# Kernel tuning notes

Measured on AMD Instinct MI355X. Metric: run time of the kernel, lower is better.

The kernel has to match this reference:

```python
import jax, jax.numpy as jnp
import numpy as np

U, V, A = 100000, 50000, 5000   # n_users, n_videos, n_vloggers
D = 64                           # latent_dim_rec
N_LAYERS = 3                     # VAGNN_n_layers
NNZ_UI, NNZ_UA, NNZ_G2, NNZ_G4 = 4_000_000, 2_000_000, 200_000, 2_000_000
BATCH = 1024

def spmm(rows, cols, vals, x, n_rows):
    # sparse.mm(COO(rows, cols, vals), x) -> [n_rows, d]
    return jax.ops.segment_sum(vals[:, None] * x[cols], rows, num_segments=n_rows)

def one_propagate(rows, cols, vals, a_feat, b_feat):
    # LightGCN propagation: mean over layer-0..n embeddings (running sum, no stack)
    n = a_feat.shape[0] + b_feat.shape[0]
    feats = jnp.concatenate([a_feat, b_feat], axis=0)
    acc, cur = feats, feats
    for _ in range(N_LAYERS):
        cur = spmm(rows, cols, vals, cur, n)
        acc = acc + cur
    light = acc / (N_LAYERS + 1)
    return light[:a_feat.shape[0]], light[a_feat.shape[0]:]

def l2norm(x):
    # F.normalize(x, dim=1), eps=1e-12
    return x / jnp.maximum(jnp.linalg.norm(x, axis=1, keepdims=True), 1e-12)

def setup_inputs() -> dict:
    key = jax.random.key(0)
    ks = jax.random.split(key, 16)
    return {
        'emb_user':    jax.random.normal(ks[0], (U, D), jnp.float32) * 0.1,
        'emb_video':   jax.random.normal(ks[1], (V, D), jnp.float32) * 0.1,
        'emb_vlogger': jax.random.normal(ks[2], (A, D), jnp.float32) * 0.1,
        'q':           jax.random.normal(ks[3], (D, D), jnp.float32) * 0.1,
        'ui_rows': jax.random.randint(ks[4], (NNZ_UI,), 0, U + V, jnp.int32),
        'ui_cols': jax.random.randint(ks[5], (NNZ_UI,), 0, U + V, jnp.int32),
        'ui_vals': jax.random.uniform(ks[6], (NNZ_UI,), jnp.float32) * 0.01,
        'ua_rows': jax.random.randint(ks[7], (NNZ_UA,), 0, U + A, jnp.int32),
        'ua_cols': jax.random.randint(ks[8], (NNZ_UA,), 0, U + A, jnp.int32),
        'ua_vals': jax.random.uniform(ks[9], (NNZ_UA,), jnp.float32) * 0.01,
        'g2_rows': jax.random.randint(ks[10], (NNZ_G2,), 0, A, jnp.int32),
        'g2_cols': jax.random.randint(ks[11], (NNZ_G2,), 0, V, jnp.int32),
        'g2_vals': jax.random.uniform(ks[12], (NNZ_G2,), jnp.float32) * 0.01,
        'g4_rows': jax.random.randint(ks[13], (NNZ_G4,), 0, V, jnp.int32),
        'g4_cols': jax.random.randint(ks[14], (NNZ_G4,), 0, U, jnp.int32),
        'g4_vals': jax.random.uniform(ks[15], (NNZ_G4,), jnp.float32) * 0.01,
        'vlogger_list': jax.random.randint(jax.random.fold_in(key, 100), (V,), 0, A, jnp.int32),
        'users': jax.random.randint(jax.random.fold_in(key, 101), (BATCH,), 0, U, jnp.int32),
    }

def reference(emb_user, emb_video, emb_vlogger, q,
              ui_rows, ui_cols, ui_vals,
              ua_rows, ua_cols, ua_vals,
              g2_rows, g2_cols, g2_vals,
              g4_rows, g4_cols, g4_vals,
              vlogger_list, users):
    # computer()
    atom_u, atom_v = one_propagate(ui_rows, ui_cols, ui_vals, emb_user, emb_video)
    atom_a = l2norm(spmm(g2_rows, g2_cols, g2_vals, atom_v, A))
    non_u, non_a = one_propagate(ua_rows, ua_cols, ua_vals, emb_user, emb_vlogger)
    non_v = l2norm(spmm(g4_rows, g4_cols, g4_vals, non_u, V))
    # getUsersRating()
    u_a, u_n = atom_u[users], non_u[users]                 # [B, D]
    vl_a, vl_n = atom_a[vlogger_list], non_a[vlogger_list]  # [V, D]
    ui = jax.nn.sigmoid(u_a @ atom_v.T + u_n @ non_v.T)      # [B, V]
    ua = jax.nn.sigmoid(u_a @ vl_a.T + u_n @ vl_n.T)         # [B, V]
    vid = (atom_v + non_v) * 0.5
    vlog = (vl_a + vl_n) * 0.5
    w = jax.nn.sigmoid(jnp.sum((vid @ q) * vlog, axis=1))    # [V]
    return w * ui + (1.0 - w) * ua
```

## Files before the change

kernel.cpp:

```cpp
#include <hip/hip_runtime.h>
#include <hip/hip_bf16.h>

#define U_N 100000
#define V_N 50000
#define A_N 5000

typedef float4 f4;
typedef unsigned int u32;
typedef __attribute__((ext_vector_type(8))) short bf16x8;
typedef __attribute__((ext_vector_type(4))) float f32x4;

__device__ inline float bflo(u32 p) { return __uint_as_float(p << 16); }
__device__ inline float bfhi(u32 p) { return __uint_as_float(p & 0xffff0000u); }
__device__ inline u32 f2bf(float f) {
  u32 u = __float_as_uint(f);
  return (u + 0x7fffu + ((u >> 16) & 1u)) >> 16;
}
__device__ inline u32 pack2(float lo, float hi) {
  return f2bf(lo) | (f2bf(hi) << 16);
}
__device__ inline bf16x8 ld8(const u32* p) {
  uint4 u = *(const uint4*)p;
  return __builtin_bit_cast(bf16x8, u);
}

__global__ void k_concat2b(const float* __restrict__ a, int na,
                           const float* __restrict__ b, int nb,
                           u32* __restrict__ curH, float* __restrict__ acc) {
  int total4 = (na + nb) * 16;
  for (int i = blockIdx.x * blockDim.x + threadIdx.x; i < total4;
       i += gridDim.x * blockDim.x) {
    int fi = i * 4;
    f4 v = (fi < na * 64) ? *(const f4*)(a + fi)
                          : *(const f4*)(b + (fi - na * 64));
    *(f4*)(acc + fi) = v;
    uint2 h; h.x = pack2(v.x, v.y); h.y = pack2(v.z, v.w);
    *(uint2*)(curH + (fi >> 1)) = h;
  }
}

__global__ void k_count(const int* __restrict__ rows, int nnz, int* __restrict__ cnt) {
  for (int i = blockIdx.x * blockDim.x + threadIdx.x; i < nnz;
       i += gridDim.x * blockDim.x)
    atomicAdd(&cnt[rows[i]], 1);
}

__global__ void k_bsum(const int* __restrict__ cnt, int n, int* __restrict__ bsum) {
  __shared__ int red[1024];
  int t = threadIdx.x;
  int i = blockIdx.x * 1024 + t;
  red[t] = (i < n) ? cnt[i] : 0;
  __syncthreads();
  for (int off = 512; off; off >>= 1) {
    if (t < off) red[t] += red[t + off];
    __syncthreads();
  }
  if (t == 0) bsum[blockIdx.x] = red[0];
}

__global__ void k_bscan(int* __restrict__ bsum, int nb) {
  if (threadIdx.x == 0) {
    int run = 0;
    for (int i = 0; i < nb; ++i) {
      int c = bsum[i];
      bsum[i] = run;
      run += c;
    }
  }
}

__global__ void k_bapply(const int* __restrict__ cnt, int n,
                         const int* __restrict__ bsum,
                         int* __restrict__ rp, int* __restrict__ pos) {
  __shared__ int sc[1024];
  int t = threadIdx.x;
  int i = blockIdx.x * 1024 + t;
  int c = (i < n) ? cnt[i] : 0;
  sc[t] = c;
  __syncthreads();
  #pragma unroll
  for (int off = 1; off < 1024; off <<= 1) {
    int v = (t >= off) ? sc[t - off] : 0;
    __syncthreads();
    sc[t] += v;
    __syncthreads();
  }
  int val = bsum[blockIdx.x] + sc[t] - c;
  if (i < n) {
    rp[i] = val;
    pos[i] = val;
    if (i == n - 1) rp[n] = val + c;
  }
}

__global__ void k_fill(const int* __restrict__ rows, const int* __restrict__ cols,
                       const float* __restrict__ vals, int nnz,
                       int* __restrict__ pos, int* __restrict__ ci,
                       float* __restrict__ cv) {
  for (int i = blockIdx.x * blockDim.x + threadIdx.x; i < nnz;
       i += gridDim.x * blockDim.x) {
    int slot = atomicAdd(&pos[rows[i]], 1);
    ci[slot] = cols[i];
    cv[slot] = vals[i];
  }
}

__global__ void k_spmm_b(const int* __restrict__ rp, const int* __restrict__ ci,
                         const float* __restrict__ cv, int nrows,
                         const u32* __restrict__ inH, int instrU,
                         u32* __restrict__ outH, int ostrU, int ocolU,
                         float* __restrict__ acc, int l2n) {
  int lane = threadIdx.x & 63;
  int w = (blockIdx.x * blockDim.x + threadIdx.x) >> 6;
  int nw = (gridDim.x * blockDim.x) >> 6;
  int eg = lane >> 3;
  int du = (lane & 7) * 4;
  for (int r = w; r < nrows; r += nw) {
    int e0 = rp[r], e1 = rp[r + 1];
    float s[8] = {0.f, 0.f, 0.f, 0.f, 0.f, 0.f, 0.f, 0.f};
    int e = e0 + eg;
    for (; e + 8 < e1; e += 16) {
      int c0 = ci[e];     float v0 = cv[e];
      int c1 = ci[e + 8]; float v1 = cv[e + 8];
      uint4 x0 = *(const uint4*)(inH + (size_t)c0 * instrU + du);
      uint4 x1 = *(const uint4*)(inH + (size_t)c1 * instrU + du);
      s[0] = fmaf(v0, bflo(x0.x), s[0]); s[1] = fmaf(v0, bfhi(x0.x), s[1]);
      s[2] = fmaf(v0, bflo(x0.y), s[2]); s[3] = fmaf(v0, bfhi(x0.y), s[3]);
      s[4] = fmaf(v0, bflo(x0.z), s[4]); s[5] = fmaf(v0, bfhi(x0.z), s[5]);
      s[6] = fmaf(v0, bflo(x0.w), s[6]); s[7] = fmaf(v0, bfhi(x0.w), s[7]);
      s[0] = fmaf(v1, bflo(x1.x), s[0]); s[1] = fmaf(v1, bfhi(x1.x), s[1]);
      s[2] = fmaf(v1, bflo(x1.y), s[2]); s[3] = fmaf(v1, bfhi(x1.y), s[3]);
      s[4] = fmaf(v1, bflo(x1.z), s[4]); s[5] = fmaf(v1, bfhi(x1.z), s[5]);
      s[6] = fmaf(v1, bflo(x1.w), s[6]); s[7] = fmaf(v1, bfhi(x1.w), s[7]);
    }
    if (e < e1) {
      int c0 = ci[e]; float v0 = cv[e];
      uint4 x0 = *(const uint4*)(inH + (size_t)c0 * instrU + du);
      s[0] = fmaf(v0, bflo(x0.x), s[0]); s[1] = fmaf(v0, bfhi(x0.x), s[1]);
      s[2] = fmaf(v0, bflo(x0.y), s[2]); s[3] = fmaf(v0, bfhi(x0.y), s[3]);
      s[4] = fmaf(v0, bflo(x0.z), s[4]); s[5] = fmaf(v0, bfhi(x0.z), s[5]);
      s[6] = fmaf(v0, bflo(x0.w), s[6]); s[7] = fmaf(v0, bfhi(x0.w), s[7]);
    }
    #pragma unroll
    for (int j = 0; j < 8; ++j) {
      s[j] += __shfl_xor(s[j], 8);
      s[j] += __shfl_xor(s[j], 16);
      s[j] += __shfl_xor(s[j], 32);
    }
    if (l2n) {
      float ss = 0.f;
      #pragma unroll
      for (int j = 0; j < 8; ++j) ss = fmaf(s[j], s[j], ss);
      ss += __shfl_xor(ss, 1);
      ss += __shfl_xor(ss, 2);
      ss += __shfl_xor(ss, 4);
      float inv = 1.0f / fmaxf(sqrtf(ss), 1e-12f);
      #pragma unroll
      for (int j = 0; j < 8; ++j) s[j] *= inv;
    }
    if (eg == 0) {
      uint4 o;
      o.x = pack2(s[0], s[1]); o.y = pack2(s[2], s[3]);
      o.z = pack2(s[4], s[5]); o.w = pack2(s[6], s[7]);
      *(uint4*)(outH + (size_t)r * ostrU + ocolU + du) = o;
      if (acc) {
        float* ap = acc + (size_t)r * 64 + (lane & 7) * 8;
        f4 a0 = *(f4*)ap, a1 = *(f4*)(ap + 4);
        a0.x += s[0]; a0.y += s[1]; a0.z += s[2]; a0.w += s[3];
        a1.x += s[4]; a1.y += s[5]; a1.z += s[6]; a1.w += s[7];
        *(f4*)ap = a0; *(f4*)(ap + 4) = a1;
      }
    }
  }
}

__global__ void k_scale_ua(float* __restrict__ acc, u32* __restrict__ UAuH) {
  int total4 = (U_N + A_N) * 16;
  for (int i = blockIdx.x * blockDim.x + threadIdx.x; i < total4;
       i += gridDim.x * blockDim.x) {
    int fi = i * 4;
    f4 v = *(f4*)(acc + fi);
    v.x *= 0.25f; v.y *= 0.25f; v.z *= 0.25f; v.w *= 0.25f;
    *(f4*)(acc + fi) = v;
    if (fi < U_N * 64) {
      uint2 h; h.x = pack2(v.x, v.y); h.y = pack2(v.z, v.w);
      *(uint2*)(UAuH + (fi >> 1)) = h;
    }
  }
}

__global__ void k_scale_ui(float* __restrict__ acc, u32* __restrict__ VAH) {
  int total4 = (U_N + V_N) * 16;
  for (int i = blockIdx.x * blockDim.x + threadIdx.x; i < total4;
       i += gridDim.x * blockDim.x) {
    int fi = i * 4;
    f4 v = *(f4*)(acc + fi);
    v.x *= 0.25f; v.y *= 0.25f; v.z *= 0.25f; v.w *= 0.25f;
    *(f4*)(acc + fi) = v;
    if (fi >= U_N * 64) {
      int rem = fi - U_N * 64;
      int row = rem >> 6, col = rem & 63;
      uint2 h; h.x = pack2(v.x, v.y); h.y = pack2(v.z, v.w);
      *(uint2*)(VAH + (size_t)row * 64 + (col >> 1)) = h;
    }
  }
}

__global__ void k_gather_u(const int* __restrict__ users,
                           const float* __restrict__ accUI,
                           const float* __restrict__ accUA,
                           u32* __restrict__ UcatH) {
  int b = blockIdx.x;
  int t = threadIdx.x;
  int u = users[b];
  UcatH[b * 64 + t] = pack2(accUI[(size_t)u * 64 + 2 * t], accUI[(size_t)u * 64 + 2 * t + 1]);
  UcatH[b * 64 + 32 + t] = pack2(accUA[(size_t)u * 64 + 2 * t], accUA[(size_t)u * 64 + 2 * t + 1]);
}

__global__ void k_gather_vb(const int* __restrict__ vlist,
                            const u32* __restrict__ atomAH,
                            const float* __restrict__ accUA,
                            u32* __restrict__ VBH) {
  int v = blockIdx.x * 4 + (threadIdx.x >> 5);
  int t = threadIdx.x & 31;
  int a = vlist[v];
  VBH[(size_t)v * 64 + t] = atomAH[(size_t)a * 32 + t];
  VBH[(size_t)v * 64 + 32 + t] =
      pack2(accUA[(size_t)(U_N + a) * 64 + 2 * t], accUA[(size_t)(U_N + a) * 64 + 2 * t + 1]);
}

__global__ void k_w(const u32* __restrict__ VAH, const u32* __restrict__ VBH,
                    const float* __restrict__ q, float* __restrict__ wv) {
  __shared__ float qs[64 * 64];
  for (int i = threadIdx.x; i < 4096; i += blockDim.x) qs[i] = q[i];
  __syncthreads();
  int lane = threadIdx.x & 63;
  int v = blockIdx.x * 4 + (threadIdx.x >> 6);
  if (v >= V_N) return;
  int half = lane & 1;
  u32 pa0 = VAH[(size_t)v * 64 + (lane >> 1)];
  u32 pa1 = VAH[(size_t)v * 64 + 32 + (lane >> 1)];
  u32 pb0 = VBH[(size_t)v * 64 + (lane >> 1)];
  u32 pb1 = VBH[(size_t)v * 64 + 32 + (lane >> 1)];
  float vid = 0.5f * ((half ? bfhi(pa0) : bflo(pa0)) + (half ? bfhi(pa1) : bflo(pa1)));
  float vlog = 0.5f * ((half ? bfhi(pb0) : bflo(pb0)) + (half ? bfhi(pb1) : bflo(pb1)));
  float s = 0.0f;
  for (int d = 0; d < 64; ++d)
    s = fmaf(__shfl(vid, d, 64), qs[d * 64 + lane], s);
  float t = s * vlog;
  #pragma unroll
  for (int off = 32; off; off >>= 1) t += __shfl_xor(t, off, 64);
  if (lane == 0) wv[v] = 1.0f / (1.0f + __expf(-t));
}

__global__ __launch_bounds__(256) void k_rating_mfma(
    const u32* __restrict__ UcatH, const u32* __restrict__ VAH,
    const u32* __restrict__ VBH, const float* __restrict__ wv,
    float* __restrict__ out) {
  int lane = threadIdx.x & 63;
  int wave = threadIdx.x >> 6;
  int n0 = blockIdx.x * 64;
  int m0 = blockIdx.y * 256 + wave * 64;
  int rr = lane & 15, g = lane >> 4;
  f32x4 accA[4][4], accB[4][4];
  #pragma unroll
  for (int i = 0; i < 4; ++i)
    #pragma unroll
    for (int j = 0; j < 4; ++j) {
      accA[i][j] = (f32x4){0.f, 0.f, 0.f, 0.f};
      accB[i][j] = (f32x4){0.f, 0.f, 0.f, 0.f};
    }
  #pragma unroll
  for (int ks = 0; ks < 4; ++ks) {
    int ko = ks * 16 + g * 4;
    bf16x8 a[4], bA[4], bB[4];
    #pragma unroll
    for (int i = 0; i < 4; ++i)
      a[i] = ld8(UcatH + (size_t)(m0 + i * 16 + rr) * 64 + ko);
    #pragma unroll
    for (int j = 0; j < 4; ++j) {
      int nr = n0 + j * 16 + rr;
      if (nr >= V_N) nr = V_N - 1;
      bA[j] = ld8(VAH + (size_t)nr * 64 + ko);
      bB[j] = ld8(VBH + (size_t)nr * 64 + ko);
    }
    #pragma unroll
    for (int i = 0; i < 4; ++i)
      #pragma unroll
      for (int j = 0; j < 4; ++j) {
        accA[i][j] = __builtin_amdgcn_mfma_f32_16x16x32_bf16(a[i], bA[j], accA[i][j], 0, 0, 0);
        accB[i][j] = __builtin_amdgcn_mfma_f32_16x16x32_bf16(a[i], bB[j], accB[i][j], 0, 0, 0);
      }
  }
  #pragma unroll
  for (int j = 0; j < 4; ++j) {
    int v = n0 + j * 16 + rr;
    if (v >= V_N) continue;
    float wvv = wv[v];
    #pragma unroll
    for (int i = 0; i < 4; ++i) {
      #pragma unroll
      for (int reg = 0; reg < 4; ++reg) {
        int u = m0 + i * 16 + g * 4 + reg;
        float sa = 1.0f / (1.0f + __expf(-accA[i][j][reg]));
        float sb = 1.0f / (1.0f + __expf(-accB[i][j][reg]));
        out[(size_t)u * V_N + v] = wvv * sa + (1.0f - wvv) * sb;
      }
    }
  }
}

extern "C" void kernel_launch(void* const* d_in, const int* in_sizes, int n_in,
                              void* d_out, int out_size, void* d_ws, size_t ws_size,
                              hipStream_t stream) {
  const float* emb_user    = (const float*)d_in[0];
  const float* emb_video   = (const float*)d_in[1];
  const float* emb_vlogger = (const float*)d_in[2];
  const float* q           = (const float*)d_in[3];
  const int*   ui_rows = (const int*)d_in[4];
  const int*   ui_cols = (const int*)d_in[5];
  const float* ui_vals = (const float*)d_in[6];
  const int*   ua_rows = (const int*)d_in[7];
  const int*   ua_cols = (const int*)d_in[8];
  const float* ua_vals = (const float*)d_in[9];
  const int*   g2_rows = (const int*)d_in[10];
  const int*   g2_cols = (const int*)d_in[11];
  const float* g2_vals = (const float*)d_in[12];
  const int*   g4_rows = (const int*)d_in[13];
  const int*   g4_cols = (const int*)d_in[14];
  const float* g4_vals = (const float*)d_in[15];
  const int*   vlist   = (const int*)d_in[16];
  const int*   users   = (const int*)d_in[17];
  int nnz_ui = in_sizes[4], nnz_ua = in_sizes[7];
  int nnz_g2 = in_sizes[10], nnz_g4 = in_sizes[13];

  float* ws = (float*)d_ws;
  float* accUI = ws;
  float* accUA = ws + 9600000;
  u32*   curH  = (u32*)(ws + 16320000);
  u32*   nxtH  = (u32*)(ws + 21120000);
  u32*   VAH   = (u32*)(ws + 25920000);
  u32*   VBH   = (u32*)(ws + 29120000);
  u32*   UAuH  = (u32*)(ws + 32320000);
  u32*   UcatH = (u32*)(ws + 35520000);
  u32*   atomAH= (u32*)(ws + 35585536);
  float* wv    = ws + 35745536;
  int*   bsum  = (int*)(ws + 35795536);
  int*   ib    = (int*)(ws + 35800000);

  const int nUI = U_N + V_N, nUA = U_N + A_N;
  auto nr_pad = [](int nrows) { return (size_t)((nrows + 1 + 15) & ~15); };

  auto build_csr = [&](const int* rows, const int* cols, const float* vals,
                       int nnz, int nrows, int* rp, int* pos, int* ci, float* cv) {
    hipMemsetAsync(pos, 0, (size_t)nrows * 4, stream);
    k_count<<<2048, 256, 0, stream>>>(rows, nnz, pos);
    int nb = (nrows + 1023) / 1024;
    k_bsum<<<nb, 1024, 0, stream>>>(pos, nrows, bsum);
    k_bscan<<<1, 64, 0, stream>>>(bsum, nb);
    k_bapply<<<nb, 1024, 0, stream>>>(pos, nrows, bsum, rp, pos);
    k_fill<<<2048, 256, 0, stream>>>(rows, cols, vals, nnz, pos, ci, cv);
  };

  {
    size_t NR = nr_pad(nUI);
    int* rp = ib; int* pos = ib + NR; int* ci = ib + 2 * NR;
    float* cv = (float*)(ci + nnz_ui);
    build_csr(ui_rows, ui_cols, ui_vals, nnz_ui, nUI, rp, pos, ci, cv);
    k_concat2b<<<2048, 256, 0, stream>>>(emb_user, U_N, emb_video, V_N, curH, accUI);
    u32* p0 = curH; u32* p1 = nxtH;
    for (int l = 0; l < 3; ++l) {
      k_spmm_b<<<2048, 256, 0, stream>>>(rp, ci, cv, nUI, p0, 32, p1, 32, 0, accUI, 0);
      u32* tmp = p0; p0 = p1; p1 = tmp;
    }
  }
  {
    size_t NR = nr_pad(nUA);
    int* rp = ib; int* pos = ib + NR; int* ci = ib + 2 * NR;
    float* cv = (float*)(ci + nnz_ua);
    build_csr(ua_rows, ua_cols, ua_vals, nnz_ua, nUA, rp, pos, ci, cv);
    k_concat2b<<<2048, 256, 0, stream>>>(emb_user, U_N, emb_vlogger, A_N, curH, accUA);
    u32* p0 = curH; u32* p1 = nxtH;
    for (int l = 0; l < 3; ++l) {
      k_spmm_b<<<2048, 256, 0, stream>>>(rp, ci, cv, nUA, p0, 32, p1, 32, 0, accUA, 0);
      u32* tmp = p0; p0 = p1; p1 = tmp;
    }
  }
  k_scale_ua<<<2048, 256, 0, stream>>>(accUA, UAuH);
  k_scale_ui<<<2048, 256, 0, stream>>>(accUI, VAH);
  size_t NR4 = nr_pad(V_N), NR2 = nr_pad(A_N);
  int* rp4 = ib; int* pos4 = ib + NR4; int* ci4 = ib + 2 * NR4;
  float* cv4 = (float*)(ci4 + nnz_g4);
  int* ib2 = (int*)(cv4 + nnz_g4);
  int* rp2 = ib2; int* pos2 = ib2 + NR2; int* ci2 = ib2 + 2 * NR2;
  float* cv2 = (float*)(ci2 + nnz_g2);
  build_csr(g4_rows, g4_cols, g4_vals, nnz_g4, V_N, rp4, pos4, ci4, cv4);
  build_csr(g2_rows, g2_cols, g2_vals, nnz_g2, A_N, rp2, pos2, ci2, cv2);
  k_spmm_b<<<2048, 256, 0, stream>>>(rp2, ci2, cv2, A_N, VAH, 64, atomAH, 32, 0, nullptr, 1);
  k_spmm_b<<<2048, 256, 0, stream>>>(rp4, ci4, cv4, V_N, UAuH, 32, VAH, 64, 32, nullptr, 1);
  k_gather_u<<<1024, 32, 0, stream>>>(users, accUI, accUA, UcatH);
  k_gather_vb<<<12500, 128, 0, stream>>>(vlist, atomAH, accUA, VBH);
  k_w<<<12500, 256, 0, stream>>>(VAH, VBH, q, wv);
  dim3 gridR((V_N + 63) / 64, 1024 / 256);
  k_rating_mfma<<<gridR, 256, 0, stream>>>(UcatH, VAH, VBH, wv, (float*)d_out);
}
```

Measured before the change: 1.679 ms.

## Pack CSR edges as int2 and prune last UI layer to needed rows

CSR column indices and values are interleaved into one int2 array, so each edge needs one load instead of two. The third UI propagation layer now computes only the video rows plus the distinct batch user rows, which are collected by a marking kernel. The last layer of each propagation also skips writing the bf16 output that nothing reads. This cuts the gather and bandwidth cost of the final layer, at the price of extra small kernels and a flag buffer that reuses VBH scratch before VBH is written.

```diff
diff --git a/kernel.cpp b/kernel.cpp
--- a/kernel.cpp
+++ b/kernel.cpp
@@ -95,83 +95,121 @@
 
 __global__ void k_fill(const int* __restrict__ rows, const int* __restrict__ cols,
                        const float* __restrict__ vals, int nnz,
-                       int* __restrict__ pos, int* __restrict__ ci,
-                       float* __restrict__ cv) {
+                       int* __restrict__ pos, int2* __restrict__ ep) {
   for (int i = blockIdx.x * blockDim.x + threadIdx.x; i < nnz;
        i += gridDim.x * blockDim.x) {
     int slot = atomicAdd(&pos[rows[i]], 1);
-    ci[slot] = cols[i];
-    cv[slot] = vals[i];
-  }
-}
-
-__global__ void k_spmm_b(const int* __restrict__ rp, const int* __restrict__ ci,
-                         const float* __restrict__ cv, int nrows,
+    ep[slot] = make_int2(cols[i], __float_as_int(vals[i]));
+  }
+}
+
+__global__ void k_mark(const int* __restrict__ users, int nb,
+                       int* __restrict__ flag, int* __restrict__ rcount,
+                       int* __restrict__ rlist) {
+  int b = blockIdx.x * blockDim.x + threadIdx.x;
+  if (b < nb) {
+    int u = users[b];
+    if (atomicExch(&flag[u], 1) == 0) {
+      int m = atomicAdd(rcount, 1);
+      rlist[m] = u;
+    }
+  }
+}
+
+__device__ __forceinline__ void spmm_row(
+    int row, const int* __restrict__ rp, const int2* __restrict__ ep,
+    const u32* __restrict__ inH, int instrU,
+    u32* __restrict__ outH, int ostrU, int ocolU,
+    float* __restrict__ acc, int l2n, int wout, int lane, int eg, int du) {
+  int e0 = rp[row], e1 = rp[row + 1];
+  float s[8] = {0.f, 0.f, 0.f, 0.f, 0.f, 0.f, 0.f, 0.f};
+  int e = e0 + eg;
+  for (; e + 8 < e1; e += 16) {
+    int2 ed0 = ep[e];
+    int2 ed1 = ep[e + 8];
+    float v0 = __int_as_float(ed0.y), v1 = __int_as_float(ed1.y);
+    uint4 x0 = *(const uint4*)(inH + (size_t)ed0.x * instrU + du);
+    uint4 x1 = *(const uint4*)(inH + (size_t)ed1.x * instrU + du);
+    s[0] = fmaf(v0, bflo(x0.x), s[0]); s[1] = fmaf(v0, bfhi(x0.x), s[1]);
+    s[2] = fmaf(v0, bflo(x0.y), s[2]); s[3] = fmaf(v0, bfhi(x0.y), s[3]);
+    s[4] = fmaf(v0, bflo(x0.z), s[4]); s[5] = fmaf(v0, bfhi(x0.z), s[5]);
+    s[6] = fmaf(v0, bflo(x0.w), s[6]); s[7] = fmaf(v0, bfhi(x0.w), s[7]);
+    s[0] = fmaf(v1, bflo(x1.x), s[0]); s[1] = fmaf(v1, bfhi(x1.x), s[1]);
+    s[2] = fmaf(v1, bflo(x1.y), s[2]); s[3] = fmaf(v1, bfhi(x1.y), s[3]);
+    s[4] = fmaf(v1, bflo(x1.z), s[4]); s[5] = fmaf(v1, bfhi(x1.z), s[5]);
+    s[6] = fmaf(v1, bflo(x1.w), s[6]); s[7] = fmaf(v1, bfhi(x1.w), s[7]);
+  }
+  if (e < e1) {
+    int2 ed0 = ep[e];
+    float v0 = __int_as_float(ed0.y);
+    uint4 x0 = *(const uint4*)(inH + (size_t)ed0.x * instrU + du);
+    s[0] = fmaf(v0, bflo(x0.x), s[0]); s[1] = fmaf(v0, bfhi(x0.x), s[1]);
+    s[2] = fmaf(v0, bflo(x0.y), s[2]); s[3] = fmaf(v0, bfhi(x0.y), s[3]);
+    s[4] = fmaf(v0, bflo(x0.z), s[4]); s[5] = fmaf(v0, bfhi(x0.z), s[5]);
+    s[6] = fmaf(v0, bflo(x0.w), s[6]); s[7] = fmaf(v0, bfhi(x0.w), s[7]);
+  }
+  #pragma unroll
+  for (int j = 0; j < 8; ++j) {
+    s[j] += __shfl_xor(s[j], 8);
+    s[j] += __shfl_xor(s[j], 16);
+    s[j] += __shfl_xor(s[j], 32);
+  }
+  if (l2n) {
+    float ss = 0.f;
+    #pragma unroll
+    for (int j = 0; j < 8; ++j) ss = fmaf(s[j], s[j], ss);
+    ss += __shfl_xor(ss, 1);
+    ss += __shfl_xor(ss, 2);
+    ss += __shfl_xor(ss, 4);
+    float inv = 1.0f / fmaxf(sqrtf(ss), 1e-12f);
+    #pragma unroll
+    for (int j = 0; j < 8; ++j) s[j] *= inv;
+  }
+  if (eg == 0) {
+    if (wout) {
+      uint4 o;
+      o.x = pack2(s[0], s[1]); o.y = pack2(s[2], s[3]);
+      o.z = pack2(s[4], s[5]); o.w = pack2(s[6], s[7]);
+      *(uint4*)(outH + (size_t)row * ostrU + ocolU + du) = o;
+    }
+    if (acc) {
+      float* ap = acc + (size_t)row * 64 + (lane & 7) * 8;
+      f4 a0 = *(f4*)ap, a1 = *(f4*)(ap + 4);
+      a0.x += s[0]; a0.y += s[1]; a0.z += s[2]; a0.w += s[3];
+      a1.x += s[4]; a1.y += s[5]; a1.z += s[6]; a1.w += s[7];
+      *(f4*)ap = a0; *(f4*)(ap + 4) = a1;
+    }
+  }
+}
+
+__global__ void k_spmm_b(const int* __restrict__ rp, const int2* __restrict__ ep,
+                         int nrows, int rbase,
                          const u32* __restrict__ inH, int instrU,
                          u32* __restrict__ outH, int ostrU, int ocolU,
-                         float* __restrict__ acc, int l2n) {
+                         float* __restrict__ acc, int l2n, int wout) {
   int lane = threadIdx.x & 63;
   int w = (blockIdx.x * blockDim.x + threadIdx.x) >> 6;
   int nw = (gridDim.x * blockDim.x) >> 6;
   int eg = lane >> 3;
   int du = (lane & 7) * 4;
-  for (int r = w; r < nrows; r += nw) {
-    int e0 = rp[r], e1 = rp[r + 1];
-    float s[8] = {0.f, 0.f, 0.f, 0.f, 0.f, 0.f, 0.f, 0.f};
-    int e = e0 + eg;
-    for (; e + 8 < e1; e += 16) {
-      int c0 = ci[e];     float v0 = cv[e];
-      int c1 = ci[e + 8]; float v1 = cv[e + 8];
-      uint4 x0 = *(const uint4*)(inH + (size_t)c0 * instrU + du);
-      uint4 x1 = *(const uint4*)(inH + (size_t)c1 * instrU + du);
-      s[0] = fmaf(v0, bflo(x0.x), s[0]); s[1] = fmaf(v0, bfhi(x0.x), s[1]);
-      s[2] = fmaf(v0, bflo(x0.y), s[2]); s[3] = fmaf(v0, bfhi(x0.y), s[3]);
-      s[4] = fmaf(v0, bflo(x0.z), s[4]); s[5] = fmaf(v0, bfhi(x0.z), s[5]);
-      s[6] = fmaf(v0, bflo(x0.w), s[6]); s[7] = fmaf(v0, bfhi(x0.w), s[7]);
-      s[0] = fmaf(v1, bflo(x1.x), s[0]); s[1] = fmaf(v1, bfhi(x1.x), s[1]);
-      s[2] = fmaf(v1, bflo(x1.y), s[2]); s[3] = fmaf(v1, bfhi(x1.y), s[3]);
-      s[4] = fmaf(v1, bflo(x1.z), s[4]); s[5] = fmaf(v1, bfhi(x1.z), s[5]);
-      s[6] = fmaf(v1, bflo(x1.w), s[6]); s[7] = fmaf(v1, bfhi(x1.w), s[7]);
-    }
-    if (e < e1) {
-      int c0 = ci[e]; float v0 = cv[e];
-      uint4 x0 = *(const uint4*)(inH + (size_t)c0 * instrU + du);
-      s[0] = fmaf(v0, bflo(x0.x), s[0]); s[1] = fmaf(v0, bfhi(x0.x), s[1]);
-      s[2] = fmaf(v0, bflo(x0.y), s[2]); s[3] = fmaf(v0, bfhi(x0.y), s[3]);
-      s[4] = fmaf(v0, bflo(x0.z), s[4]); s[5] = fmaf(v0, bfhi(x0.z), s[5]);
-      s[6] = fmaf(v0, bflo(x0.w), s[6]); s[7] = fmaf(v0, bfhi(x0.w), s[7]);
-    }
-    #pragma unroll
-    for (int j = 0; j < 8; ++j) {
-      s[j] += __shfl_xor(s[j], 8);
-      s[j] += __shfl_xor(s[j], 16);
-      s[j] += __shfl_xor(s[j], 32);
-    }
-    if (l2n) {
-      float ss = 0.f;
-      #pragma unroll
-      for (int j = 0; j < 8; ++j) ss = fmaf(s[j], s[j], ss);
-      ss += __shfl_xor(ss, 1);
-      ss += __shfl_xor(ss, 2);
-      ss += __shfl_xor(ss, 4);
-      float inv = 1.0f / fmaxf(sqrtf(ss), 1e-12f);
-      #pragma unroll
-      for (int j = 0; j < 8; ++j) s[j] *= inv;
-    }
-    if (eg == 0) {
-      uint4 o;
-      o.x = pack2(s[0], s[1]); o.y = pack2(s[2], s[3]);
-      o.z = pack2(s[4], s[5]); o.w = pack2(s[6], s[7]);
-      *(uint4*)(outH + (size_t)r * ostrU + ocolU + du) = o;
-      if (acc) {
-        float* ap = acc + (size_t)r * 64 + (lane & 7) * 8;
-        f4 a0 = *(f4*)ap, a1 = *(f4*)(ap + 4);
-        a0.x += s[0]; a0.y += s[1]; a0.z += s[2]; a0.w += s[3];
-        a1.x += s[4]; a1.y += s[5]; a1.z += s[6]; a1.w += s[7];
-        *(f4*)ap = a0; *(f4*)(ap + 4) = a1;
-      }
-    }
-  }
+  for (int r = w; r < nrows; r += nw)
+    spmm_row(rbase + r, rp, ep, inH, instrU, outH, ostrU, ocolU, acc, l2n, wout,
+             lane, eg, du);
+}
+
+__global__ void k_spmm_b_list(const int* __restrict__ rp, const int2* __restrict__ ep,
+                              const int* __restrict__ rlist, const int* __restrict__ rcount,
+                              const u32* __restrict__ inH, int instrU,
+                              float* __restrict__ acc) {
+  int lane = threadIdx.x & 63;
+  int w = (blockIdx.x * blockDim.x + threadIdx.x) >> 6;
+  int nw = (gridDim.x * blockDim.x) >> 6;
+  int eg = lane >> 3;
+  int du = (lane & 7) * 4;
+  int m = *rcount;
+  for (int r = w; r < m; r += nw)
+    spmm_row(rlist[r], rp, ep, inH, instrU, nullptr, 0, 0, acc, 0, 0,
+             lane, eg, du);
 }
 
 __global__ void k_scale_ua(float* __restrict__ acc, u32* __restrict__ UAuH) {
@@ -347,57 +385,55 @@
   float* wv    = ws + 35745536;
   int*   bsum  = (int*)(ws + 35795536);
   int*   ib    = (int*)(ws + 35800000);
+  int*   flag   = (int*)VBH;
+  int*   rcount = flag + 100000;
+  int*   rlist  = flag + 100016;
 
   const int nUI = U_N + V_N, nUA = U_N + A_N;
   auto nr_pad = [](int nrows) { return (size_t)((nrows + 1 + 15) & ~15); };
 
   auto build_csr = [&](const int* rows, const int* cols, const float* vals,
-                       int nnz, int nrows, int* rp, int* pos, int* ci, float* cv) {
+                       int nnz, int nrows, int* rp, int* pos, int2* ep) {
     hipMemsetAsync(pos, 0, (size_t)nrows * 4, stream);
     k_count<<<2048, 256, 0, stream>>>(rows, nnz, pos);
     int nb = (nrows + 1023) / 1024;
     k_bsum<<<nb, 1024, 0, stream>>>(pos, nrows, bsum);
     k_bscan<<<1, 64, 0, stream>>>(bsum, nb);
     k_bapply<<<nb, 1024, 0, stream>>>(pos, nrows, bsum, rp, pos);
-    k_fill<<<2048, 256, 0, stream>>>(rows, cols, vals, nnz, pos, ci, cv);
+    k_fill<<<2048, 256, 0, stream>>>(rows, cols, vals, nnz, pos, ep);
   };
 
   {
     size_t NR = nr_pad(nUI);
-    int* rp = ib; int* pos = ib + NR; int* ci = ib + 2 * NR;
-    float* cv = (float*)(ci + nnz_ui);
-    build_csr(ui_rows, ui_cols, ui_vals, nnz_ui, nUI, rp, pos, ci, cv);
+    int* rp = ib; int* pos = ib + NR; int2* ep = (int2*)(ib + 2 * NR);
+    build_csr(ui_rows, ui_cols, ui_vals, nnz_ui, nUI, rp, pos, ep);
     k_concat2b<<<2048, 256, 0, stream>>>(emb_user, U_N, emb_video, V_N, curH, accUI);
-    u32* p0 = curH; u32* p1 = nxtH;
-    for (int l = 0; l < 3; ++l) {
-      k_spmm_b<<<2048, 256, 0, stream>>>(rp, ci, cv, nUI, p0, 32, p1, 32, 0, accUI, 0);
-      u32* tmp = p0; p0 = p1; p1 = tmp;
-    }
+    hipMemsetAsync(flag, 0, (size_t)(100016) * 4, stream);
+    k_mark<<<4, 256, 0, stream>>>(users, 1024, flag, rcount, rlist);
+    k_spmm_b<<<2048, 256, 0, stream>>>(rp, ep, nUI, 0, curH, 32, nxtH, 32, 0, accUI, 0, 1);
+    k_spmm_b<<<2048, 256, 0, stream>>>(rp, ep, nUI, 0, nxtH, 32, curH, 32, 0, accUI, 0, 1);
+    k_spmm_b<<<2048, 256, 0, stream>>>(rp, ep, V_N, U_N, curH, 32, nullptr, 0, 0, accUI, 0, 0);
+    k_spmm_b_list<<<16, 256, 0, stream>>>(rp, ep, rlist, rcount, curH, 32, accUI);
   }
   {
     size_t NR = nr_pad(nUA);
-    int* rp = ib; int* pos = ib + NR; int* ci = ib + 2 * NR;
-    float* cv = (float*)(ci + nnz_ua);
-    build_csr(ua_rows, ua_cols, ua_vals, nnz_ua, nUA, rp, pos, ci, cv);
+    int* rp = ib; int* pos = ib + NR; int2* ep = (int2*)(ib + 2 * NR);
+    build_csr(ua_rows, ua_cols, ua_vals, nnz_ua, nUA, rp, pos, ep);
     k_concat2b<<<2048, 256, 0, stream>>>(emb_user, U_N, emb_vlogger, A_N, curH, accUA);
-    u32* p0 = curH; u32* p1 = nxtH;
-    for (int l = 0; l < 3; ++l) {
-      k_spmm_b<<<2048, 256, 0, stream>>>(rp, ci, cv, nUA, p0, 32, p1, 32, 0, accUA, 0);
-      u32* tmp = p0; p0 = p1; p1 = tmp;
-    }
+    k_spmm_b<<<2048, 256, 0, stream>>>(rp, ep, nUA, 0, curH, 32, nxtH, 32, 0, accUA, 0, 1);
+    k_spmm_b<<<2048, 256, 0, stream>>>(rp, ep, nUA, 0, nxtH, 32, curH, 32, 0, accUA, 0, 1);
+    k_spmm_b<<<2048, 256, 0, stream>>>(rp, ep, nUA, 0, curH, 32, nullptr, 0, 0, accUA, 0, 0);
   }
   k_scale_ua<<<2048, 256, 0, stream>>>(accUA, UAuH);
   k_scale_ui<<<2048, 256, 0, stream>>>(accUI, VAH);
   size_t NR4 = nr_pad(V_N), NR2 = nr_pad(A_N);
-  int* rp4 = ib; int* pos4 = ib + NR4; int* ci4 = ib + 2 * NR4;
-  float* cv4 = (float*)(ci4 + nnz_g4);
-  int* ib2 = (int*)(cv4 + nnz_g4);
-  int* rp2 = ib2; int* pos2 = ib2 + NR2; int* ci2 = ib2 + 2 * NR2;
-  float* cv2 = (float*)(ci2 + nnz_g2);
-  build_csr(g4_rows, g4_cols, g4_vals, nnz_g4, V_N, rp4, pos4, ci4, cv4);
-  build_csr(g2_rows, g2_cols, g2_vals, nnz_g2, A_N, rp2, pos2, ci2, cv2);
-  k_spmm_b<<<2048, 256, 0, stream>>>(rp2, ci2, cv2, A_N, VAH, 64, atomAH, 32, 0, nullptr, 1);
-  k_spmm_b<<<2048, 256, 0, stream>>>(rp4, ci4, cv4, V_N, UAuH, 32, VAH, 64, 32, nullptr, 1);
+  int* rp4 = ib; int* pos4 = ib + NR4; int2* ep4 = (int2*)(ib + 2 * NR4);
+  int* ib2 = (int*)(ep4 + nnz_g4);
+  int* rp2 = ib2; int* pos2 = ib2 + NR2; int2* ep2 = (int2*)(ib2 + 2 * NR2);
+  build_csr(g4_rows, g4_cols, g4_vals, nnz_g4, V_N, rp4, pos4, ep4);
+  build_csr(g2_rows, g2_cols, g2_vals, nnz_g2, A_N, rp2, pos2, ep2);
+  k_spmm_b<<<2048, 256, 0, stream>>>(rp2, ep2, A_N, 0, VAH, 64, atomAH, 32, 0, nullptr, 1, 1);
+  k_spmm_b<<<2048, 256, 0, stream>>>(rp4, ep4, V_N, 0, UAuH, 32, VAH, 64, 32, nullptr, 1, 1);
   k_gather_u<<<1024, 32, 0, stream>>>(users, accUI, accUA, UcatH);
   k_gather_vb<<<12500, 128, 0, stream>>>(vlist, atomAH, accUA, VBH);
   k_w<<<12500, 256, 0, stream>>>(VAH, VBH, q, wv);
```

Result: slower. 1.720 ms (+2.5%).
